# Kernel optimization log

Measured on AMD Instinct MI355X. Metric: run time of the kernel, lower is better.

The kernel has to match this reference:

```python
import jax, jax.numpy as jnp
import numpy as np

# ---- static config (mirrors YOLOH_Expand cfg) ----
H, W = 200, 200            # feature map size
A = 9                      # num_anchors
C = 80                     # num_classes
M = H * W * A              # total anchors
K = 1000                   # topk NMS candidates
STRIDE = 16
CTR_CLAMP = 32.0
CONF_THRESH = 0.05
NMS_THRESH = 0.6
SCALE_CLAMP = float(np.log(1000.0 / 16))  # DEFAULT_SCALE_CLAMP
ANCHOR_SIZES = np.array([[32,32],[64,64],[128,128],[32,64],[64,32],
                         [64,128],[128,64],[128,256],[256,128]], dtype=np.float32)


def make_anchors():
    # generate_anchors: meshgrid (+0.5)*stride centers, tiled anchor sizes -> (M,4) cxcywh
    ys, xs = np.meshgrid(np.arange(H), np.arange(W), indexing='ij')
    xy = (np.stack([xs, ys], -1).reshape(-1, 2).astype(np.float32) + 0.5) * STRIDE  # (HW,2)
    xy = np.repeat(xy[:, None, :], A, axis=1)                                       # (HW,A,2)
    wh = np.broadcast_to(ANCHOR_SIZES[None], (H * W, A, 2)).astype(np.float32)
    return jnp.asarray(np.concatenate([xy, wh], -1).reshape(-1, 4))


def setup_inputs() -> dict:
    key = jax.random.key(0)
    k1, k2 = jax.random.split(key)
    return {
        'cls_pred': jax.random.normal(k1, (1, M, C), jnp.float32) - 2.0,  # logits, mostly low conf
        'reg_pred': jax.random.normal(k2, (1, M, 4), jnp.float32) * 0.5,
        'anchor_boxes': make_anchors(),
    }


def decode_boxes(anchors, reg):
    # decode_boxes: clamped center offset + clamped log-scale wh -> x1y1x2y2
    ctr_off = jnp.clip(reg[..., :2] * anchors[..., 2:], -CTR_CLAMP, CTR_CLAMP)
    ctr_xy = anchors[..., :2] + ctr_off
    dwdh = jnp.minimum(reg[..., 2:], SCALE_CLAMP)
    wh = anchors[..., 2:] * jnp.exp(dwdh)
    return jnp.concatenate([ctr_xy - 0.5 * wh, ctr_xy + 0.5 * wh], axis=-1)


def pairwise_iou(b):
    # exact math of YOLOH_Expand.nms
    x1, y1, x2, y2 = b[:, 0], b[:, 1], b[:, 2], b[:, 3]
    areas = (x2 - x1) * (y2 - y1)
    xx1 = jnp.maximum(x1[:, None], x1[None, :])
    yy1 = jnp.maximum(y1[:, None], y1[None, :])
    xx2 = jnp.minimum(x2[:, None], x2[None, :])
    yy2 = jnp.minimum(y2[:, None], y2[None, :])
    w = jnp.maximum(1e-28, xx2 - xx1)
    h = jnp.maximum(1e-28, yy2 - yy1)
    inter = w * h
    return inter / (areas[:, None] + areas[None, :] - inter + 1e-14)


def greedy_nms_keep(iou, cls_ids, valid):
    # per-class greedy NMS over score-sorted candidates: box i is suppressed if
    # any kept higher-score box j of the same class has IoU > thresh.
    same = cls_ids[:, None] == cls_ids[None, :]           # (K,K)
    idx = jnp.arange(K)

    def body(keep, i):
        prior = idx < i
        sup = jnp.any(keep & prior & same[i] & (iou[i] > NMS_THRESH))
        keep = keep.at[i].set((~sup) & valid[i])
        return keep, None

    keep0 = jnp.zeros((K,), dtype=bool)
    keep, _ = jax.lax.scan(body, keep0, idx)
    return keep


def reference(cls_pred, reg_pred, anchor_boxes):
    scores = jax.nn.sigmoid(cls_pred[0])                  # (M,C)
    boxes = decode_boxes(anchor_boxes, reg_pred[0])       # (M,4)
    # postprocess: per-anchor best class + confidence threshold
    cls_inds = jnp.argmax(scores, axis=1)                 # (M,)
    sc = jnp.max(scores, axis=1)                          # (M,)
    valid = sc >= CONF_THRESH
    # fixed-size top-k candidate set (invalid ranked last)
    _, top_i = jax.lax.top_k(jnp.where(valid, sc, -1.0), K)
    b = boxes[top_i]                                      # (K,4)
    s = sc[top_i]                                         # (K,)
    c = cls_inds[top_i]                                   # (K,)
    v = valid[top_i]                                      # (K,)
    iou = pairwise_iou(b)                                 # (K,K)
    keep = greedy_nms_keep(iou, c, v)                     # (K,) bool
    return b, s * keep.astype(s.dtype), c.astype(jnp.int32), keep
```

## Files before the change

kernel.cpp:

```cpp
#include <hip/hip_runtime.h>
#include <math.h>

typedef unsigned long long u64;
typedef unsigned int u32;

#define M_ANCH 360000
#define NCLS 80
#define KTOP 1000
#define CAP 8192
#define NBINS 65536
#define RREP 8
#define CONF_THRESH 0.05f
#define NMS_THRESH 0.6f
#define CTR_CLAMP 32.0f
#define SCALE_CLAMP 4.1351665567423560f

#define AS1 __attribute__((address_space(1)))
#define AS3 __attribute__((address_space(3)))

#define HIST_OFF   0u
#define HIST_BYTES (RREP * NBINS * 4u)
#define CNT_OFF    (HIST_OFF + HIST_BYTES)
#define B_OFF      (CNT_OFF + 4u)
#define VW_OFF     (B_OFF + 4u + 8u)
#define ZERO_END   (VW_OFF + 128u)
#define MERGED_OFF ZERO_END
#define BLKSUM_OFF (MERGED_OFF + NBINS * 4u)
#define CAND_OFF   (BLKSUM_OFF + 256u)
#define SC_OFF     (CAND_OFF + CAP * 8u)
#define CLS_OFF    (SC_OFF + M_ANCH * 4u)
#define SSC_OFF    (CLS_OFF + M_ANCH * 4u)
#define SCLS_OFF   (SSC_OFF + KTOP * 4u)
#define SUP_OFF    ((SCLS_OFF + KTOP * 4u + 15u) & ~15u)

__device__ __forceinline__ u32 fkey(float f) {
    u32 u = __float_as_uint(f);
    return (u & 0x80000000u) ? ~u : (u | 0x80000000u);
}

__global__ __launch_bounds__(256) void k_score(const float* __restrict__ cls_pred,
                                               float* __restrict__ sc_all,
                                               int* __restrict__ cls_all,
                                               u32* __restrict__ hist) {
    __shared__ float4 stage[1280];
    int t = threadIdx.x;
    const float4* gp = (const float4*)cls_pred + (size_t)blockIdx.x * 1280;
#pragma unroll
    for (int k = 0; k < 5; k++) {
        int f = t + 256 * k;
        __builtin_amdgcn_global_load_lds((AS1 void*)(gp + f),
                                         (AS3 void*)(stage + f), 16, 0, 0);
    }
    __syncthreads();

    if (t < 64) {
        const float4* av = stage + t * 20;
        float mv = -1e30f; int mc = 0;
        int k0 = t & 7;
#pragma unroll
        for (int i = 0; i < 20; i++) {
            int k = k0 + i;
            if (k >= 20) k -= 20;
            float4 v = av[k];
            float lm_ = v.x; int lc_ = 4 * k;
            if (v.y > lm_) { lm_ = v.y; lc_ = 4 * k + 1; }
            if (v.z > lm_) { lm_ = v.z; lc_ = 4 * k + 2; }
            if (v.w > lm_) { lm_ = v.w; lc_ = 4 * k + 3; }
            if (lm_ > mv || (lm_ == mv && lc_ < mc)) { mv = lm_; mc = lc_; }
        }
        int a = blockIdx.x * 64 + t;
        float sc = 1.0f / (1.0f + expf(-mv));
        sc_all[a] = sc;
        cls_all[a] = mc;
        float msk = (sc >= CONF_THRESH) ? sc : -1.0f;
        u32 u = fkey(msk);
        atomicAdd(&hist[((blockIdx.x & (RREP - 1)) << 16) + (u >> 16)], 1u);
    }
}

__global__ __launch_bounds__(1024) void k_hsum(const u32* __restrict__ hist,
                                               u32* __restrict__ merged,
                                               u32* __restrict__ blksum) {
    __shared__ u32 red[1024];
    int t = threadIdx.x;
    int b = blockIdx.x * 1024 + t;
    u32 s = 0;
#pragma unroll
    for (int r = 0; r < RREP; r++) s += hist[r * NBINS + b];
    merged[b] = s;
    red[t] = s;
    __syncthreads();
    for (int off = 512; off > 0; off >>= 1) {
        if (t < off) red[t] += red[t + off];
        __syncthreads();
    }
    if (t == 0) blksum[blockIdx.x] = red[0];
}

__global__ __launch_bounds__(1024) void k_boundary(const u32* __restrict__ merged,
                                                   const u32* __restrict__ blksum,
                                                   u32* __restrict__ outB) {
    __shared__ u32 bs[64];
    __shared__ u32 sj, sA;
    __shared__ u32 csum[1024];
    int t = threadIdx.x;
    if (t < 64) bs[t] = blksum[t];
    __syncthreads();
    if (t == 0) {
        u32 cum = 0; u32 j = 0; u32 Aj = 0;
        for (int b = 63; b >= 0; b--) {
            if (cum + bs[b] >= KTOP) { j = (u32)b; Aj = cum; break; }
            cum += bs[b];
        }
        sj = j; sA = Aj;
    }
    __syncthreads();
    u32 j = sj, Aj = sA;
    u32 h = merged[j * 1024 + t];
    csum[t] = h;
    __syncthreads();
    u32 v = h;
    for (int off = 1; off < 1024; off <<= 1) {
        u32 add = (t + off < 1024) ? csum[t + off] : 0u;
        __syncthreads();
        v += add;
        csum[t] = v;
        __syncthreads();
    }
    u32 above = (t == 1023) ? 0u : csum[t + 1];
    if (Aj + above < KTOP && Aj + above + h >= KTOP) outB[0] = j * 1024 + t;
}

__global__ __launch_bounds__(256) void k_compact(const float* __restrict__ sc_all,
                                                 const u32* __restrict__ pB,
                                                 u32* __restrict__ counter,
                                                 u64* __restrict__ cand) {
    int i = blockIdx.x * 256 + threadIdx.x;
    if (i >= M_ANCH) return;
    u32 B = *pB;
    float s = sc_all[i];
    float m = (s >= CONF_THRESH) ? s : -1.0f;
    u32 u = fkey(m);
    if ((u >> 16) >= B) {
        u32 pos = atomicAdd(counter, 1u);
        if (pos < CAP) cand[pos] = ((u64)u << 32) | (u64)(0xFFFFFFFFu - (u32)i);
    }
}

__global__ __launch_bounds__(1024) void k_select(const u64* __restrict__ cand,
                                                 const u32* __restrict__ counter,
                                                 const float* __restrict__ sc_all,
                                                 const int* __restrict__ cls_all,
                                                 const float* __restrict__ reg_pred,
                                                 const float* __restrict__ anchors,
                                                 float* __restrict__ out,
                                                 float* __restrict__ sel_sc,
                                                 int* __restrict__ sel_cls,
                                                 u64* __restrict__ valid_words) {
    __shared__ u64 keys[CAP];
    int t = threadIdx.x;
    u32 n = *counter;
    if (n > CAP) n = CAP;
    u32 P = 1024;
    while (P < n) P <<= 1;
    for (u32 i = t; i < P; i += 1024) keys[i] = (i < n) ? cand[i] : 0ull;
    for (u32 k = 2; k <= P; k <<= 1) {
        for (u32 j = k >> 1; j > 0; j >>= 1) {
            __syncthreads();
            for (u32 i = t; i < P; i += 1024) {
                u32 ixj = i ^ j;
                if (ixj > i) {
                    u64 a = keys[i], b = keys[ixj];
                    bool desc = ((i & k) == 0);
                    if (desc ? (a < b) : (a > b)) { keys[i] = b; keys[ixj] = a; }
                }
            }
        }
    }
    __syncthreads();
    if (t < KTOP) {
        u64 key = keys[t];
        u32 idx = 0xFFFFFFFFu - (u32)(key & 0xFFFFFFFFull);
        if (idx >= M_ANCH) idx = 0;
        float s = sc_all[idx];
        int cl = cls_all[idx];
        float4 a = ((const float4*)anchors)[idx];
        float4 r = ((const float4*)reg_pred)[idx];
        float ox = fminf(fmaxf(r.x * a.z, -CTR_CLAMP), CTR_CLAMP);
        float oy = fminf(fmaxf(r.y * a.w, -CTR_CLAMP), CTR_CLAMP);
        float cx = a.x + ox, cy = a.y + oy;
        float ww = a.z * expf(fminf(r.z, SCALE_CLAMP));
        float hh = a.w * expf(fminf(r.w, SCALE_CLAMP));
        float4 box;
        box.x = cx - 0.5f * ww;
        box.y = cy - 0.5f * hh;
        box.z = cx + 0.5f * ww;
        box.w = cy + 0.5f * hh;
        ((float4*)out)[t] = box;
        out[5 * KTOP + t] = (float)cl;
        sel_sc[t] = s;
        sel_cls[t] = cl;
        if (s >= CONF_THRESH) atomicOr(&valid_words[t >> 6], 1ull << (t & 63));
    }
}

__global__ __launch_bounds__(256) void k_supmat(const float* __restrict__ out,
                                                const int* __restrict__ sel_cls,
                                                u64* __restrict__ sup) {
    int wid = threadIdx.x >> 6;
    int lane = threadIdx.x & 63;
    int g = blockIdx.x * 4 + wid;
    int i = g >> 4;
    int w = g & 15;
    int j = w * 64 + lane;
    int jc = (j < KTOP) ? j : (KTOP - 1);
    float4 bi = ((const float4*)out)[i];
    float4 bj = ((const float4*)out)[jc];
    int ci = sel_cls[i], cj = sel_cls[jc];
    float ai = (bi.z - bi.x) * (bi.w - bi.y);
    float aj = (bj.z - bj.x) * (bj.w - bj.y);
    float xx1 = fmaxf(bi.x, bj.x), yy1 = fmaxf(bi.y, bj.y);
    float xx2 = fminf(bi.z, bj.z), yy2 = fminf(bi.w, bj.w);
    float iw = fmaxf(1e-28f, xx2 - xx1), ih = fmaxf(1e-28f, yy2 - yy1);
    float inter = iw * ih;
    float iou = inter / (ai + aj - inter + 1e-14f);
    bool pred = (j < i) && (ci == cj) && (iou > NMS_THRESH);
    u64 bal = __ballot((int)pred);
    if (lane == 0) sup[g] = bal;
}

__global__ __launch_bounds__(64) void k_nms(const u64* __restrict__ sup,
                                            const u64* __restrict__ valid_words,
                                            const float* __restrict__ sel_sc,
                                            float* __restrict__ out) {
    __shared__ u64 keepA[16];
    int lane = threadIdx.x;
    if (lane < 16) keepA[lane] = 0ull;
    __syncthreads();

    for (int b = 0; b < 16; b++) {
        int row = b * 64 + lane;
        int rowc = (row < KTOP) ? row : (KTOP - 1);
        const ulonglong2* rp = (const ulonglong2*)(sup + (size_t)rowc * 16);
        ulonglong2 q0 = rp[0], q1 = rp[1], q2 = rp[2], q3 = rp[3];
        ulonglong2 q4 = rp[4], q5 = rp[5], q6 = rp[6], q7 = rp[7];
        u64 d = sup[(size_t)rowc * 16 + b];
        u64 vm = valid_words[b];

        u64 acc = (q0.x & keepA[0])  | (q0.y & keepA[1])
                | (q1.x & keepA[2])  | (q1.y & keepA[3])
                | (q2.x & keepA[4])  | (q2.y & keepA[5])
                | (q3.x & keepA[6])  | (q3.y & keepA[7])
                | (q4.x & keepA[8])  | (q4.y & keepA[9])
                | (q5.x & keepA[10]) | (q5.y & keepA[11])
                | (q6.x & keepA[12]) | (q6.y & keepA[13])
                | (q7.x & keepA[14]) | (q7.y & keepA[15]);
        u64 premask = __ballot(acc != 0ull);
        u64 eligible = vm & ~premask;

        u32 dlo = (u32)d, dhi = (u32)(d >> 32);
        u64 kb = 0ull;
#pragma unroll
        for (int j = 0; j < 64; j++) {
            u32 djl = __builtin_amdgcn_readlane(dlo, j);
            u32 djh = __builtin_amdgcn_readlane(dhi, j);
            u64 dj = ((u64)djh << 32) | (u64)djl;
            bool kj = (((eligible >> j) & 1ull) != 0ull) && ((dj & kb) == 0ull);
            kb |= ((u64)(kj ? 1u : 0u)) << j;
        }
        if (lane == 0) keepA[b] = kb;
        __syncthreads();
    }

    for (int t = lane; t < KTOP; t += 64) {
        int kb = (int)((keepA[t >> 6] >> (t & 63)) & 1ull);
        float s = sel_sc[t];
        out[4 * KTOP + t] = kb ? s : 0.0f;
        out[6 * KTOP + t] = (float)kb;
    }
}

extern "C" void kernel_launch(void* const* d_in, const int* in_sizes, int n_in,
                              void* d_out, int out_size, void* d_ws, size_t ws_size,
                              hipStream_t stream) {
    const float* cls_pred = (const float*)d_in[0];
    const float* reg_pred = (const float*)d_in[1];
    const float* anchors  = (const float*)d_in[2];
    float* out = (float*)d_out;
    char* ws = (char*)d_ws;

    u32* hist     = (u32*)(ws + HIST_OFF);
    u32* counter  = (u32*)(ws + CNT_OFF);
    u32* pB       = (u32*)(ws + B_OFF);
    u64* vwords   = (u64*)(ws + VW_OFF);
    u32* merged   = (u32*)(ws + MERGED_OFF);
    u32* blksum   = (u32*)(ws + BLKSUM_OFF);
    u64* cand     = (u64*)(ws + CAND_OFF);
    float* sc_all = (float*)(ws + SC_OFF);
    int* cls_all  = (int*)(ws + CLS_OFF);
    float* sel_sc = (float*)(ws + SSC_OFF);
    int* sel_cls  = (int*)(ws + SCLS_OFF);
    u64* sup      = (u64*)(ws + SUP_OFF);

    hipMemsetAsync(d_ws, 0, ZERO_END, stream);

    int nbs = M_ANCH / 64;
    int nbc = (M_ANCH + 255) / 256;
    k_score<<<nbs, 256, 0, stream>>>(cls_pred, sc_all, cls_all, hist);
    k_hsum<<<NBINS / 1024, 1024, 0, stream>>>(hist, merged, blksum);
    k_boundary<<<1, 1024, 0, stream>>>(merged, blksum, pB);
    k_compact<<<nbc, 256, 0, stream>>>(sc_all, pB, counter, cand);
    k_select<<<1, 1024, 0, stream>>>(cand, counter, sc_all, cls_all, reg_pred,
                                     anchors, out, sel_sc, sel_cls, vwords);
    k_supmat<<<(KTOP * 16) / 4, 256, 0, stream>>>(out, sel_cls, sup);
    k_nms<<<1, 64, 0, stream>>>(sup, vwords, sel_sc, out);
}
```

Measured before the change: 316.0 us.

## Persistent double-buffered score kernel with all-thread argmax and separate histogram pass

The score kernel becomes persistent with a grid of 1024 blocks. Each block walks its tiles and prefetches the next tile into a second LDS buffer through global_load_lds while it processes the current one. All 256 threads now take part in the per-anchor argmax: four lanes each scan a quarter of the classes and merge results with a packed key via shuffles, where before only 64 threads did the work. The histogram atomics move out into a new vectorized k_hist kernel that rereads sc_all, which adds one extra launch and one small read pass in exchange for overlapped loads and better lane utilization.

Measured after the change: 353.4 us. 1.12x slower.

```diff
diff --git a/kernel.cpp b/kernel.cpp
--- a/kernel.cpp
+++ b/kernel.cpp
@@ -33,34 +33,61 @@
 #define SCLS_OFF   (SSC_OFF + KTOP * 4u)
 #define SUP_OFF    ((SCLS_OFF + KTOP * 4u + 15u) & ~15u)
 
+#define NTILES 5625
+#define SCORE_GRID 1024
+
 __device__ __forceinline__ u32 fkey(float f) {
     u32 u = __float_as_uint(f);
     return (u & 0x80000000u) ? ~u : (u | 0x80000000u);
 }
+__device__ __forceinline__ float unfkey(u32 u) {
+    u32 f = (u & 0x80000000u) ? (u & 0x7FFFFFFFu) : ~u;
+    return __uint_as_float(f);
+}
 
 __global__ __launch_bounds__(256) void k_score(const float* __restrict__ cls_pred,
                                                float* __restrict__ sc_all,
-                                               int* __restrict__ cls_all,
-                                               u32* __restrict__ hist) {
-    __shared__ float4 stage[1280];
-    int t = threadIdx.x;
-    const float4* gp = (const float4*)cls_pred + (size_t)blockIdx.x * 1280;
-#pragma unroll
-    for (int k = 0; k < 5; k++) {
-        int f = t + 256 * k;
-        __builtin_amdgcn_global_load_lds((AS1 void*)(gp + f),
-                                         (AS3 void*)(stage + f), 16, 0, 0);
-    }
-    __syncthreads();
-
-    if (t < 64) {
-        const float4* av = stage + t * 20;
+                                               int* __restrict__ cls_all) {
+    __shared__ float4 stage[2][1280];
+    const int t = threadIdx.x;
+    const int w = t >> 6;
+    const int l = t & 63;
+    const int q = l >> 2;
+    const int p = l & 3;
+
+    int tile = blockIdx.x;
+    {
+        const float4* gp = (const float4*)cls_pred + (size_t)tile * 1280;
+#pragma unroll
+        for (int k = 0; k < 5; k++) {
+            int f = t + 256 * k;
+            __builtin_amdgcn_global_load_lds((AS1 void*)(gp + f),
+                                             (AS3 void*)(&stage[0][f]), 16, 0, 0);
+        }
+    }
+    int cur = 0;
+    for (; tile < NTILES; tile += SCORE_GRID) {
+        int next = tile + SCORE_GRID;
+        if (next < NTILES) {
+            const float4* gp = (const float4*)cls_pred + (size_t)next * 1280;
+#pragma unroll
+            for (int k = 0; k < 5; k++) {
+                int f = t + 256 * k;
+                __builtin_amdgcn_global_load_lds((AS1 void*)(gp + f),
+                                                 (AS3 void*)(&stage[cur ^ 1][f]), 16, 0, 0);
+            }
+            asm volatile("s_waitcnt vmcnt(5)" ::: "memory");
+        } else {
+            asm volatile("s_waitcnt vmcnt(0)" ::: "memory");
+        }
+        __builtin_amdgcn_s_barrier();
+        __builtin_amdgcn_sched_barrier(0);
+
+        const float4* av = &stage[cur][(16 * w + q) * 20];
         float mv = -1e30f; int mc = 0;
-        int k0 = t & 7;
-#pragma unroll
-        for (int i = 0; i < 20; i++) {
-            int k = k0 + i;
-            if (k >= 20) k -= 20;
+#pragma unroll
+        for (int i = 0; i < 5; i++) {
+            int k = 5 * p + ((i + q) % 5);
             float4 v = av[k];
             float lm_ = v.x; int lc_ = 4 * k;
             if (v.y > lm_) { lm_ = v.y; lc_ = 4 * k + 1; }
@@ -68,14 +95,33 @@
             if (v.w > lm_) { lm_ = v.w; lc_ = 4 * k + 3; }
             if (lm_ > mv || (lm_ == mv && lc_ < mc)) { mv = lm_; mc = lc_; }
         }
-        int a = blockIdx.x * 64 + t;
-        float sc = 1.0f / (1.0f + expf(-mv));
-        sc_all[a] = sc;
-        cls_all[a] = mc;
-        float msk = (sc >= CONF_THRESH) ? sc : -1.0f;
-        u32 u = fkey(msk);
-        atomicAdd(&hist[((blockIdx.x & (RREP - 1)) << 16) + (u >> 16)], 1u);
-    }
+        u64 key = ((u64)fkey(mv) << 32) | (u64)(~(u32)mc);
+        u64 o = __shfl_xor(key, 1); if (o > key) key = o;
+        o = __shfl_xor(key, 2);     if (o > key) key = o;
+        if (p == 0) {
+            int a = tile * 64 + 16 * w + q;
+            float lv = unfkey((u32)(key >> 32));
+            float sc = 1.0f / (1.0f + expf(-lv));
+            sc_all[a] = sc;
+            cls_all[a] = (int)(~(u32)key);
+        }
+        __builtin_amdgcn_s_barrier();
+        __builtin_amdgcn_sched_barrier(0);
+        cur ^= 1;
+    }
+}
+
+__global__ __launch_bounds__(256) void k_hist(const float* __restrict__ sc_all,
+                                              u32* __restrict__ hist) {
+    int i4 = blockIdx.x * 256 + threadIdx.x;
+    if (i4 >= M_ANCH / 4) return;
+    float4 s4 = ((const float4*)sc_all)[i4];
+    u32 rep = ((u32)blockIdx.x & (RREP - 1)) << 16;
+    float m;
+    m = (s4.x >= CONF_THRESH) ? s4.x : -1.0f; atomicAdd(&hist[rep + (fkey(m) >> 16)], 1u);
+    m = (s4.y >= CONF_THRESH) ? s4.y : -1.0f; atomicAdd(&hist[rep + (fkey(m) >> 16)], 1u);
+    m = (s4.z >= CONF_THRESH) ? s4.z : -1.0f; atomicAdd(&hist[rep + (fkey(m) >> 16)], 1u);
+    m = (s4.w >= CONF_THRESH) ? s4.w : -1.0f; atomicAdd(&hist[rep + (fkey(m) >> 16)], 1u);
 }
 
 __global__ __launch_bounds__(1024) void k_hsum(const u32* __restrict__ hist,
@@ -304,9 +350,9 @@
 
     hipMemsetAsync(d_ws, 0, ZERO_END, stream);
 
-    int nbs = M_ANCH / 64;
     int nbc = (M_ANCH + 255) / 256;
-    k_score<<<nbs, 256, 0, stream>>>(cls_pred, sc_all, cls_all, hist);
+    k_score<<<SCORE_GRID, 256, 0, stream>>>(cls_pred, sc_all, cls_all);
+    k_hist<<<(M_ANCH / 4 + 255) / 256, 256, 0, stream>>>(sc_all, hist);
     k_hsum<<<NBINS / 1024, 1024, 0, stream>>>(hist, merged, blksum);
     k_boundary<<<1, 1024, 0, stream>>>(merged, blksum, pB);
     k_compact<<<nbc, 256, 0, stream>>>(sc_all, pB, counter, cand);
```
